# Kernel tuning notes

Hardware: AMD Instinct MI355X
Metric: run time of the kernel (lower is better)

Reference implementation:

```python
import jax, jax.numpy as jnp
import numpy as np

E = 8            # num experts
D = 1024         # hidden size
F = 4096         # ffn hidden size
CAP_FACTOR = 2.0 # expert-choice capacity factor


def setup_inputs() -> dict:
    key = jax.random.key(0)
    ks = jax.random.split(key, 6)
    B, S = 8, 1024
    hidden_states = jax.random.normal(ks[0], (B, S, D), dtype=jnp.float32)
    Wg = jax.random.normal(ks[1], (D, E), dtype=jnp.float32) * (1.0 / np.sqrt(D))
    W1 = jax.random.normal(ks[2], (E, D, F), dtype=jnp.float32) * (1.0 / np.sqrt(D))
    b1 = jnp.zeros((E, F), dtype=jnp.float32)
    W2 = jax.random.normal(ks[3], (E, F, D), dtype=jnp.float32) * (1.0 / np.sqrt(F))
    b2 = jnp.zeros((E, D), dtype=jnp.float32)
    return {"hidden_states": hidden_states, "Wg": Wg, "W1": W1, "b1": b1,
            "W2": W2, "b2": b2}


def reference(hidden_states, Wg, W1, b1, W2, b2):
    B, S, d = hidden_states.shape
    T = B * S
    C = int(T * CAP_FACTOR / E)  # capacity per expert (static)

    x = hidden_states.reshape(T, d)                      # [T, D]
    gates = jax.nn.softmax(x @ Wg, axis=-1)              # [T, E] router probs

    # Expert-choice routing: each expert picks its top-C tokens.
    scores = gates.T                                     # [E, T]
    top_vals, idx = jax.lax.top_k(scores, C)             # [E, C]

    # Load-balancing aux loss (mean gate prob * fraction routed, per expert).
    frac_routed = jnp.zeros((T, E), gates.dtype).at[
        idx.reshape(-1), jnp.repeat(jnp.arange(E), C)].set(1.0).mean(axis=0)
    aux_loss = E * jnp.sum(gates.mean(axis=0) * frac_routed)

    # Grouped expert FFN on gathered tokens.
    xg = x[idx]                                          # [E, C, D]
    h = jax.nn.gelu(jnp.einsum('ecd,edf->ecf', xg, W1) + b1[:, None, :])
    yo = jnp.einsum('ecf,efd->ecd', h, W2) + b2[:, None, :]  # [E, C, D]

    # Weight by routing prob and scatter-add back to token positions.
    weighted = yo * top_vals[..., None]                  # [E, C, D]
    out = jnp.zeros((T, d), x.dtype).at[idx.reshape(-1)].add(
        weighted.reshape(-1, d))
    return out.reshape(B, S, d), aux_loss
```

## Files before the change

kernel.cpp:

```cpp
#include <hip/hip_runtime.h>
#include <hip/hip_bf16.h>

#define T_TOK 8192
#define E_EXP 8
#define D_HID 1024
#define F_FFN 4096
#define C_CAP 2048

typedef __attribute__((ext_vector_type(8))) short bf16x8;
typedef __attribute__((ext_vector_type(4))) float f32x4;

__device__ __forceinline__ void load_lds16(const void* g, void* l) {
    __builtin_amdgcn_global_load_lds(
        (const __attribute__((address_space(1))) unsigned int*)g,
        (__attribute__((address_space(3))) unsigned int*)l, 16, 0, 0);
}

__device__ __forceinline__ float gelu_fast(float v) {
    float z = v * (1.5957691216057308f + 0.07135481627f * v * v);
    return v / (1.0f + __expf(-z));
}

__global__ __launch_bounds__(256) void gating_kernel(
    const float* __restrict__ x, const float* __restrict__ Wg,
    float* __restrict__ gatesT, __hip_bfloat16* __restrict__ xbf,
    float* __restrict__ aux_out)
{
    const int token = blockIdx.x * 4 + (threadIdx.x >> 6);
    const int lane  = threadIdx.x & 63;
    if (token == 0 && lane == 0)
        aux_out[0] = (float)E_EXP * (float)C_CAP / (float)T_TOK;
    const float* xr = x + (size_t)token * D_HID;

    float acc[E_EXP];
#pragma unroll
    for (int e = 0; e < E_EXP; ++e) acc[e] = 0.0f;

#pragma unroll
    for (int it = 0; it < 4; ++it) {
        const int c4 = it * 64 + lane;
        float4 v = ((const float4*)xr)[c4];
        float vv[4] = {v.x, v.y, v.z, v.w};
        union { __hip_bfloat16 h[4]; short4 s; } u;
#pragma unroll
        for (int j = 0; j < 4; ++j) u.h[j] = __float2bfloat16(vv[j]);
        ((short4*)(xbf + (size_t)token * D_HID))[c4] = u.s;
        const float* wr0 = Wg + (size_t)c4 * 4 * E_EXP;
#pragma unroll
        for (int j = 0; j < 4; ++j)
#pragma unroll
            for (int e = 0; e < E_EXP; ++e) acc[e] += vv[j] * wr0[j * E_EXP + e];
    }
#pragma unroll
    for (int e = 0; e < E_EXP; ++e) {
        for (int off = 32; off; off >>= 1) acc[e] += __shfl_down(acc[e], off);
    }
    if (lane == 0) {
        float m = acc[0];
#pragma unroll
        for (int e = 1; e < E_EXP; ++e) m = fmaxf(m, acc[e]);
        float ex[E_EXP];
        float s = 0.0f;
#pragma unroll
        for (int e = 0; e < E_EXP; ++e) { ex[e] = expf(acc[e] - m); s += ex[e]; }
        float inv = 1.0f / s;
#pragma unroll
        for (int e = 0; e < E_EXP; ++e) gatesT[(size_t)e * T_TOK + token] = ex[e] * inv;
    }
}

__global__ __launch_bounds__(1024) void topk_kernel(
    const float* __restrict__ gatesT, int* __restrict__ topidx,
    float* __restrict__ topval, int* __restrict__ cnt, int* __restrict__ inv)
{
    __shared__ unsigned int hist[256];
    __shared__ unsigned int bc_v, bc_r;
    __shared__ unsigned int selcnt;

    const int e    = blockIdx.x;
    const int tid  = threadIdx.x;
    const int lane = tid & 63;
    const float* row = gatesT + (size_t)e * T_TOK;

    unsigned long long kreg[8];
#pragma unroll
    for (int p = 0; p < 8; ++p) {
        int i = tid + p * 1024;
        unsigned int b = __float_as_uint(row[i]);
        b = (b & 0x80000000u) ? ~b : (b | 0x80000000u);
        kreg[p] = ((unsigned long long)b << 32) | (unsigned int)(T_TOK - 1 - i);
    }
    if (tid == 0) selcnt = 0;

    unsigned long long prefix = 0ull, mask = 0ull;
    unsigned int rank = C_CAP;
    for (int byte = 7; byte >= 0; --byte) {
        if (tid < 256) hist[tid] = 0;
        __syncthreads();
        const int sh = byte * 8;
#pragma unroll
        for (int p = 0; p < 8; ++p) {
            unsigned long long k = kreg[p];
            if ((k & mask) == prefix)
                atomicAdd(&hist[(unsigned int)((k >> sh) & 255ull)], 1u);
        }
        __syncthreads();
        if (tid < 64) {
            unsigned int v0 = hist[tid * 4], v1 = hist[tid * 4 + 1];
            unsigned int v2 = hist[tid * 4 + 2], v3 = hist[tid * 4 + 3];
            unsigned int s3 = v3, s2 = v2 + s3, s1 = v1 + s2, s0 = v0 + s1;
            unsigned int t = s0;
#pragma unroll
            for (int off = 1; off < 64; off <<= 1) {
                unsigned int u = __shfl_down(t, off);
                if (lane + off < 64) t += u;
            }
            const unsigned int suf = t - s0;
            unsigned int ge[4] = {s0 + suf, s1 + suf, s2 + suf, s3 + suf};
            unsigned int gt[4] = {s1 + suf, s2 + suf, s3 + suf, suf};
#pragma unroll
            for (int j = 0; j < 4; ++j)
                if (ge[j] >= rank && gt[j] < rank) {
                    bc_v = (unsigned int)(tid * 4 + j); bc_r = rank - gt[j];
                }
        }
        __syncthreads();
        prefix |= ((unsigned long long)bc_v) << sh;
        mask   |= (0xFFull << sh);
        rank = bc_r;
        __syncthreads();
    }
    const unsigned long long thr = prefix;

#pragma unroll
    for (int p = 0; p < 8; ++p) {
        unsigned long long k = kreg[p];
        if (k >= thr) {
            int c = (int)atomicAdd(&selcnt, 1u);
            int idx = T_TOK - 1 - (int)(k & 0xFFFFFFFFull);
            unsigned int b = (unsigned int)(k >> 32);
            b = (b & 0x80000000u) ? (b & 0x7FFFFFFFu) : ~b;
            topidx[e * C_CAP + c] = idx;
            topval[e * C_CAP + c] = __uint_as_float(b);
            int slot = atomicAdd(&cnt[idx], 1);
            inv[idx * E_EXP + slot] = e * C_CAP + c;
        }
    }
}

__global__ __launch_bounds__(256) void transpose_bf16_kernel(
    const float* __restrict__ in, __hip_bfloat16* __restrict__ out,
    int R, int Cn)
{
    __shared__ float tile[64][65];
    const int e = blockIdx.z;
    in  += (size_t)e * R * Cn;
    out += (size_t)e * R * Cn;
    const int c0 = blockIdx.x * 64, r0 = blockIdx.y * 64;
    const int tid = threadIdx.x;

    const int lr = tid >> 4, lc4 = (tid & 15) * 4;
#pragma unroll
    for (int it = 0; it < 4; ++it) {
        int r = lr + it * 16;
        float4 v = *(const float4*)(in + (size_t)(r0 + r) * Cn + c0 + lc4);
        tile[r][lc4 + 0] = v.x; tile[r][lc4 + 1] = v.y;
        tile[r][lc4 + 2] = v.z; tile[r][lc4 + 3] = v.w;
    }
    __syncthreads();

    const int ocb = tid >> 3, j0 = (tid & 7) * 8;
#pragma unroll
    for (int it = 0; it < 2; ++it) {
        int oc = ocb + it * 32;
        union { __hip_bfloat16 h[8]; uint4 v; } u;
#pragma unroll
        for (int j = 0; j < 8; ++j) u.h[j] = __float2bfloat16(tile[j0 + j][oc]);
        *(uint4*)(out + (size_t)(c0 + oc) * R + r0 + j0) = u.v;
    }
}


#define BARS do { __builtin_amdgcn_s_barrier(); __builtin_amdgcn_sched_barrier(0); } while (0)
#define WLG  do { asm volatile("s_waitcnt lgkmcnt(0)" ::: "memory"); __builtin_amdgcn_sched_barrier(0); } while (0)
#define VMC4 asm volatile("s_waitcnt vmcnt(4)" ::: "memory")
#define VMC0 asm volatile("s_waitcnt vmcnt(0)" ::: "memory")

#define STG2_A(hh, s) do { int b_ = (((s) & 1) << 15) + ((hh) << 14) + (w << 10); \
    load_lds16(Abase + (size_t)(aog[hh][0] + (s) * 128), smem + b_); \
    load_lds16(Abase + (size_t)(aog[hh][1] + (s) * 128), smem + b_ + 8192); } while (0)
#define STG2_B(hh, s) do { int b_ = 65536 + (((s) & 1) << 15) + ((hh) << 14) + (w << 10); \
    load_lds16(Bbase + (size_t)(bog[hh][0] + (s) * 128), smem + b_); \
    load_lds16(Bbase + (size_t)(bog[hh][1] + (s) * 128), smem + b_ + 8192); } while (0)

#define STG1_A(hh, s) do { int b_ = (((s) & 1) << 15) + ((hh) << 14) + (w << 10); \
    int o_ = ((s) & 15) * 128; \
    load_lds16(Abase + (size_t)(aog[hh][0] + o_), smem + b_); \
    load_lds16(Abase + (size_t)(aog[hh][1] + o_), smem + b_ + 8192); } while (0)
#define STG1_B(hh, s) do { int b_ = 65536 + (((s) & 1) << 15) + ((hh) << 14) + (w << 10); \
    int o_ = ((s) >> 4) * 524288 + ((s) & 15) * 128; \
    load_lds16(Bbase + (size_t)(bog[hh][0] + o_), smem + b_); \
    load_lds16(Bbase + (size_t)(bog[hh][1] + o_), smem + b_ + 8192); } while (0)

#define READ_A(mh) do { _Pragma("unroll") for (int mi = 0; mi < 4; ++mi) { \
    aF[mi][0] = *(const bf16x8*)(Ab + (arow + (mh) * 8192 + mi * 2048 + kc0)); \
    aF[mi][1] = *(const bf16x8*)(Ab + (arow + (mh) * 8192 + mi * 2048 + kc1)); } } while (0)
#define READ_B(nh, dst) do { _Pragma("unroll") for (int ni = 0; ni < 2; ++ni) { \
    dst[ni][0] = *(const bf16x8*)(Bb + (brow + (nh) * 4096 + ni * 2048 + kc0)); \
    dst[ni][1] = *(const bf16x8*)(Bb + (brow + (nh) * 4096 + ni * 2048 + kc1)); } } while (0)

#define QUAD(mh, nh, BF) do { \
    __builtin_amdgcn_s_setprio(1); \
    _Pragma("unroll") for (int mi = 0; mi < 4; ++mi) \
    _Pragma("unroll") for (int ni = 0; ni < 2; ++ni) { \
        acc[(mh)*4+mi][(nh)*2+ni] = __builtin_amdgcn_mfma_f32_16x16x32_bf16( \
            aF[mi][0], BF[ni][0], acc[(mh)*4+mi][(nh)*2+ni], 0, 0, 0); \
        acc[(mh)*4+mi][(nh)*2+ni] = __builtin_amdgcn_mfma_f32_16x16x32_bf16( \
            aF[mi][1], BF[ni][1], acc[(mh)*4+mi][(nh)*2+ni], 0, 0, 0); } \
    __builtin_amdgcn_s_setprio(0); } while (0)

#define GEMM_PROLOGUE_G(SA, SB) do { \
    SA(0, 0); SA(1, 0); SB(0, 0); SB(1, 0); \
    SB(0, 1); SB(1, 1); \
    VMC4; BARS; } while (0)

#define GEMM_TILE_G(t, NT, SA, SB) do { \
    const char* Ab = smem + (((t) & 1) << 15); \
    const char* Bb = smem + 65536 + (((t) & 1) << 15); \
     \
    READ_A(0); READ_B(0, bF0); \
    if ((t) + 1 < (NT)) SA(0, (t) + 1); \
    BARS; WLG; QUAD(0, 0, bF0); BARS; \
     \
    READ_B(1, bF1); \
    if ((t) + 1 < (NT)) SA(1, (t) + 1); \
    BARS; WLG; QUAD(0, 1, bF1); BARS; \
     \
    READ_A(1); \
    if ((t) + 2 < (NT)) SB(0, (t) + 2); \
    BARS; WLG; QUAD(1, 1, bF1); BARS; \
     \
    if ((t) + 2 < (NT)) SB(1, (t) + 2); \
    BARS; WLG; QUAD(1, 0, bF0); \
    if ((t) + 2 < (NT)) { VMC4; } else { VMC0; } \
    BARS; } while (0)

__global__ __launch_bounds__(512, 2) void gemm1_kernel(
    const __hip_bfloat16* __restrict__ xb,
    const __hip_bfloat16* __restrict__ W1t,
    const float* __restrict__ b1,
    const int* __restrict__ topidx,
    __hip_bfloat16* __restrict__ hbuf)
{
    __shared__ __align__(16) char smem[131072];
    const int tid = threadIdx.x;
    const int w = tid >> 6, lane = tid & 63;
    const int wr = w >> 2, wc = w & 3;
    const int fr = lane & 15, qlane = lane >> 4;

    const int bid = blockIdx.x;
    const int wg  = (bid & 7) * 32 + (bid >> 3);
    const int nc  = wg & 3;
    const int m0  = ((wg >> 2) & 7) * 256;
    const int e   = wg >> 5;
    const int nc0 = nc * 1024;

    const char* Abase = (const char*)xb;
    const char* Bbase = (const char*)(W1t + (size_t)e * F_FFN * D_HID);

    const int cc = (tid & 7) ^ ((tid >> 3) & 7);
    int aog[2][2], bog[2][2];
#pragma unroll
    for (int hh = 0; hh < 2; ++hh)
#pragma unroll
        for (int j = 0; j < 2; ++j) {
            int r   = m0 + hh * 128 + j * 64 + (tid >> 3);
            int tok = topidx[e * C_CAP + r];
            aog[hh][j] = (tok * D_HID + cc * 8) * 2;
            int n = nc0 + hh * 128 + j * 64 + (tid >> 3);
            bog[hh][j] = (n * D_HID + cc * 8) * 2;
        }

    float b1all[4][4];
#pragma unroll
    for (int p = 0; p < 4; ++p)
#pragma unroll
        for (int ni = 0; ni < 4; ++ni)
            b1all[p][ni] = b1[e * F_FFN + nc0 + p * 256 + wc * 64 + ni * 16 + fr];

    const int arow = (wr * 128 + fr) * 128;
    const int brow = (wc * 64 + fr) * 128;
    const int kc0  = ((qlane)     ^ (lane & 7)) * 16;
    const int kc1  = ((4 + qlane) ^ (lane & 7)) * 16;

    bf16x8 aF[4][2], bF0[2][2], bF1[2][2];
    f32x4 acc[8][4];
#pragma unroll
    for (int mi = 0; mi < 8; ++mi)
#pragma unroll
        for (int ni = 0; ni < 4; ++ni) acc[mi][ni] = (f32x4){0.f, 0.f, 0.f, 0.f};

    GEMM_PROLOGUE_G(STG1_A, STG1_B);
    const int q4 = qlane * 4;
#pragma unroll 1
    for (int p = 0; p < 4; ++p) {
#pragma unroll 2
        for (int tl = 0; tl < 16; ++tl) {
            const int t = p * 16 + tl;
            GEMM_TILE_G(t, 64, STG1_A, STG1_B);
        }
        const int n0p = nc0 + p * 256;
#pragma unroll
        for (int mi = 0; mi < 8; ++mi) {
#pragma unroll
            for (int r = 0; r < 4; ++r) {
                size_t row = (size_t)e * C_CAP + m0 + wr * 128 + mi * 16 + q4 + r;
                __hip_bfloat16* orow = hbuf + row * F_FFN + n0p + wc * 64;
#pragma unroll
                for (int ni = 0; ni < 4; ++ni)
                    orow[ni * 16 + fr] =
                        __float2bfloat16(gelu_fast(acc[mi][ni][r] + b1all[p][ni]));
            }
#pragma unroll
            for (int ni = 0; ni < 4; ++ni) acc[mi][ni] = (f32x4){0.f, 0.f, 0.f, 0.f};
        }
    }
}

__global__ __launch_bounds__(512, 2) void gemm2_kernel(
    const __hip_bfloat16* __restrict__ hbuf,
    const __hip_bfloat16* __restrict__ W2t,
    const float* __restrict__ b2,
    const float* __restrict__ topval,
    float* __restrict__ yo)
{
    __shared__ __align__(16) char smem[131072];
    const int tid = threadIdx.x;
    const int w = tid >> 6, lane = tid & 63;
    const int wr = w >> 2, wc = w & 3;
    const int fr = lane & 15, qlane = lane >> 4;

    const int bid = blockIdx.x;
    const int wg  = (bid & 7) * 32 + (bid >> 3);
    const int n0  = (wg & 3) * 256;
    const int m0  = ((wg >> 2) & 7) * 256;
    const int e   = wg >> 5;

    const char* Abase = (const char*)(hbuf + (size_t)e * C_CAP * F_FFN);
    const char* Bbase = (const char*)(W2t + (size_t)e * D_HID * F_FFN);

    const int cc = (tid & 7) ^ ((tid >> 3) & 7);
    int aog[2][2], bog[2][2];
#pragma unroll
    for (int hh = 0; hh < 2; ++hh)
#pragma unroll
        for (int j = 0; j < 2; ++j) {
            int r = m0 + hh * 128 + j * 64 + (tid >> 3);
            aog[hh][j] = (r * F_FFN + cc * 8) * 2;
            int n = n0 + hh * 128 + j * 64 + (tid >> 3);
            bog[hh][j] = (n * F_FFN + cc * 8) * 2;
        }

    const int arow = (wr * 128 + fr) * 128;
    const int brow = (wc * 64 + fr) * 128;
    const int kc0  = ((qlane)     ^ (lane & 7)) * 16;
    const int kc1  = ((4 + qlane) ^ (lane & 7)) * 16;

    bf16x8 aF[4][2], bF0[2][2], bF1[2][2];
    f32x4 acc[8][4];
#pragma unroll
    for (int mi = 0; mi < 8; ++mi)
#pragma unroll
        for (int ni = 0; ni < 4; ++ni) acc[mi][ni] = (f32x4){0.f, 0.f, 0.f, 0.f};

    GEMM_PROLOGUE_G(STG2_A, STG2_B);
#pragma unroll 2
    for (int t = 0; t < 64; ++t) GEMM_TILE_G(t, 64, STG2_A, STG2_B);

    const int q4 = qlane * 4;
    float b2v[4];
#pragma unroll
    for (int ni = 0; ni < 4; ++ni)
        b2v[ni] = b2[e * D_HID + n0 + wc * 64 + ni * 16 + fr];
#pragma unroll
    for (int mi = 0; mi < 8; ++mi) {
#pragma unroll
        for (int r = 0; r < 4; ++r) {
            const int row = m0 + wr * 128 + mi * 16 + q4 + r;
            const float g = topval[e * C_CAP + row];
            float* orow = yo + ((size_t)e * C_CAP + row) * D_HID + n0 + wc * 64;
#pragma unroll
            for (int ni = 0; ni < 4; ++ni)
                orow[ni * 16 + fr] = (acc[mi][ni][r] + b2v[ni]) * g;
        }
    }
}

__global__ __launch_bounds__(256) void combine_kernel(
    const float* __restrict__ yo, const int* __restrict__ cnt,
    const int* __restrict__ inv, float* __restrict__ out)
{
    const int t = blockIdx.x;
    const int n = cnt[t];
    const int c4 = threadIdx.x * 4;
    float4 a = {0.f, 0.f, 0.f, 0.f};
    for (int k = 0; k < n; ++k) {
        int ec = inv[t * E_EXP + k];
        float4 v = *(const float4*)(yo + (size_t)ec * D_HID + c4);
        a.x += v.x; a.y += v.y; a.z += v.z; a.w += v.w;
    }
    *(float4*)(out + (size_t)t * D_HID + c4) = a;
}

extern "C" void kernel_launch(void* const* d_in, const int* in_sizes, int n_in,
                              void* d_out, int out_size, void* d_ws, size_t ws_size,
                              hipStream_t stream) {
    const float* x  = (const float*)d_in[0];
    const float* Wg = (const float*)d_in[1];
    const float* W1 = (const float*)d_in[2];
    const float* b1 = (const float*)d_in[3];
    const float* W2 = (const float*)d_in[4];
    const float* b2 = (const float*)d_in[5];
    float* out = (float*)d_out;

    char* p = (char*)d_ws;
    float* gatesT = (float*)p;            p += (size_t)E_EXP * T_TOK * 4;
    int*   topidx = (int*)p;              p += (size_t)E_EXP * C_CAP * 4;
    float* topval = (float*)p;            p += (size_t)E_EXP * C_CAP * 4;
    int*   cnt    = (int*)p;              p += (size_t)T_TOK * 4;
    int*   inv    = (int*)p;              p += (size_t)T_TOK * E_EXP * 4;
    __hip_bfloat16* x_bf = (__hip_bfloat16*)p;  p += (size_t)T_TOK * D_HID * 2;
    __hip_bfloat16* W1t  = (__hip_bfloat16*)p;  p += (size_t)E_EXP * D_HID * F_FFN * 2;
    __hip_bfloat16* W2t  = (__hip_bfloat16*)p;  p += (size_t)E_EXP * D_HID * F_FFN * 2;
    __hip_bfloat16* hbuf = (__hip_bfloat16*)p;  p += (size_t)E_EXP * C_CAP * F_FFN * 2;
    float* yo = (float*)W1t;

    hipMemsetAsync(cnt, 0, (size_t)T_TOK * 4, stream);

    gating_kernel<<<T_TOK / 4, 256, 0, stream>>>(
        x, Wg, gatesT, x_bf, out + (size_t)T_TOK * D_HID);
    topk_kernel<<<E_EXP, 1024, 0, stream>>>(gatesT, topidx, topval, cnt, inv);

    {
        dim3 g(F_FFN / 64, D_HID / 64, E_EXP);
        transpose_bf16_kernel<<<g, 256, 0, stream>>>(W1, W1t, D_HID, F_FFN);
    }
    {
        dim3 g(D_HID / 64, F_FFN / 64, E_EXP);
        transpose_bf16_kernel<<<g, 256, 0, stream>>>(W2, W2t, F_FFN, D_HID);
    }

    gemm1_kernel<<<256, 512, 0, stream>>>(x_bf, W1t, b1, topidx, hbuf);
    gemm2_kernel<<<256, 512, 0, stream>>>(hbuf, W2t, b2, topval, yo);
    combine_kernel<<<T_TOK, 256, 0, stream>>>(yo, cnt, inv, out);
}
```

Baseline: 664.7 us.

## Triple-buffer A tiles, retile gemm1 to 256x256 blocks, merge weight transposes

The GEMM pipeline now keeps three A-tile LDS slots and two B slots (160KB LDS), prefetching A two k-steps ahead and waiting with vmcnt(8) instead of vmcnt(4). gemm1 changes from 256 blocks each covering 1024 output columns to 1024 blocks of 256x256. Its epilogue stages the GELU output through swizzled LDS so hbuf is written with coalesced 16-byte stores. The two weight-transpose launches are merged into one. The larger LDS footprint may lower occupancy, and gemm1 gets more blocks with a shorter K loop each.

```diff
diff --git a/kernel.cpp b/kernel.cpp
--- a/kernel.cpp
+++ b/kernel.cpp
@@ -149,14 +149,23 @@
 }
 
 __global__ __launch_bounds__(256) void transpose_bf16_kernel(
-    const float* __restrict__ in, __hip_bfloat16* __restrict__ out,
-    int R, int Cn)
+    const float* __restrict__ W1, __hip_bfloat16* __restrict__ W1t,
+    const float* __restrict__ W2, __hip_bfloat16* __restrict__ W2t)
 {
     __shared__ float tile[64][65];
-    const int e = blockIdx.z;
-    in  += (size_t)e * R * Cn;
-    out += (size_t)e * R * Cn;
-    const int c0 = blockIdx.x * 64, r0 = blockIdx.y * 64;
+    const int z = blockIdx.z;
+    const float* in;
+    __hip_bfloat16* out;
+    int R, Cn, c0, r0;
+    if (z < 8) {
+        R = D_HID; Cn = F_FFN;
+        in = W1 + (size_t)z * R * Cn; out = W1t + (size_t)z * R * Cn;
+        c0 = blockIdx.x * 64; r0 = blockIdx.y * 64;
+    } else {
+        R = F_FFN; Cn = D_HID;
+        in = W2 + (size_t)(z - 8) * R * Cn; out = W2t + (size_t)(z - 8) * R * Cn;
+        c0 = blockIdx.y * 64; r0 = blockIdx.x * 64;
+    }
     const int tid = threadIdx.x;
 
     const int lr = tid >> 4, lc4 = (tid & 15) * 4;
@@ -183,24 +192,16 @@
 
 #define BARS do { __builtin_amdgcn_s_barrier(); __builtin_amdgcn_sched_barrier(0); } while (0)
 #define WLG  do { asm volatile("s_waitcnt lgkmcnt(0)" ::: "memory"); __builtin_amdgcn_sched_barrier(0); } while (0)
+#define VMC8 asm volatile("s_waitcnt vmcnt(8)" ::: "memory")
 #define VMC4 asm volatile("s_waitcnt vmcnt(4)" ::: "memory")
 #define VMC0 asm volatile("s_waitcnt vmcnt(0)" ::: "memory")
 
-#define STG2_A(hh, s) do { int b_ = (((s) & 1) << 15) + ((hh) << 14) + (w << 10); \
+#define STG_A3(hh, s, slot) do { int b_ = (slot) * 32768 + ((hh) << 14) + (w << 10); \
     load_lds16(Abase + (size_t)(aog[hh][0] + (s) * 128), smem + b_); \
     load_lds16(Abase + (size_t)(aog[hh][1] + (s) * 128), smem + b_ + 8192); } while (0)
-#define STG2_B(hh, s) do { int b_ = 65536 + (((s) & 1) << 15) + ((hh) << 14) + (w << 10); \
+#define STG_B3(hh, s) do { int b_ = 98304 + (((s) & 1) << 15) + ((hh) << 14) + (w << 10); \
     load_lds16(Bbase + (size_t)(bog[hh][0] + (s) * 128), smem + b_); \
     load_lds16(Bbase + (size_t)(bog[hh][1] + (s) * 128), smem + b_ + 8192); } while (0)
-
-#define STG1_A(hh, s) do { int b_ = (((s) & 1) << 15) + ((hh) << 14) + (w << 10); \
-    int o_ = ((s) & 15) * 128; \
-    load_lds16(Abase + (size_t)(aog[hh][0] + o_), smem + b_); \
-    load_lds16(Abase + (size_t)(aog[hh][1] + o_), smem + b_ + 8192); } while (0)
-#define STG1_B(hh, s) do { int b_ = 65536 + (((s) & 1) << 15) + ((hh) << 14) + (w << 10); \
-    int o_ = ((s) >> 4) * 524288 + ((s) & 15) * 128; \
-    load_lds16(Bbase + (size_t)(bog[hh][0] + o_), smem + b_); \
-    load_lds16(Bbase + (size_t)(bog[hh][1] + o_), smem + b_ + 8192); } while (0)
 
 #define READ_A(mh) do { _Pragma("unroll") for (int mi = 0; mi < 4; ++mi) { \
     aF[mi][0] = *(const bf16x8*)(Ab + (arow + (mh) * 8192 + mi * 2048 + kc0)); \
@@ -219,30 +220,31 @@
             aF[mi][1], BF[ni][1], acc[(mh)*4+mi][(nh)*2+ni], 0, 0, 0); } \
     __builtin_amdgcn_s_setprio(0); } while (0)
 
-#define GEMM_PROLOGUE_G(SA, SB) do { \
-    SA(0, 0); SA(1, 0); SB(0, 0); SB(1, 0); \
-    SB(0, 1); SB(1, 1); \
+#define GEMM_PROLOGUE_3B() do { \
+    STG_A3(0, 0, 0); STG_A3(1, 0, 0); STG_A3(0, 1, 1); STG_A3(1, 1, 1); \
+    STG_B3(0, 0); STG_B3(1, 0); STG_B3(0, 1); STG_B3(1, 1); \
     VMC4; BARS; } while (0)
 
-#define GEMM_TILE_G(t, NT, SA, SB) do { \
-    const char* Ab = smem + (((t) & 1) << 15); \
-    const char* Bb = smem + 65536 + (((t) & 1) << 15); \
+#define GEMM_TILE_3B(t, NT) do { \
+    const char* Ab = smem + ((t) % 3) * 32768; \
+    const char* Bb = smem + 98304 + (((t) & 1) << 15); \
+    const int sl2_ = ((t) + 2) % 3; \
      \
     READ_A(0); READ_B(0, bF0); \
-    if ((t) + 1 < (NT)) SA(0, (t) + 1); \
+    if ((t) + 2 < (NT)) STG_A3(0, (t) + 2, sl2_); \
     BARS; WLG; QUAD(0, 0, bF0); BARS; \
      \
     READ_B(1, bF1); \
-    if ((t) + 1 < (NT)) SA(1, (t) + 1); \
+    if ((t) + 2 < (NT)) STG_A3(1, (t) + 2, sl2_); \
     BARS; WLG; QUAD(0, 1, bF1); BARS; \
      \
     READ_A(1); \
-    if ((t) + 2 < (NT)) SB(0, (t) + 2); \
+    if ((t) + 2 < (NT)) STG_B3(0, (t) + 2); \
     BARS; WLG; QUAD(1, 1, bF1); BARS; \
      \
-    if ((t) + 2 < (NT)) SB(1, (t) + 2); \
+    if ((t) + 2 < (NT)) STG_B3(1, (t) + 2); \
     BARS; WLG; QUAD(1, 0, bF0); \
-    if ((t) + 2 < (NT)) { VMC4; } else { VMC0; } \
+    if ((t) + 2 < (NT)) { VMC8; } else { VMC0; } \
     BARS; } while (0)
 
 __global__ __launch_bounds__(512, 2) void gemm1_kernel(
@@ -252,18 +254,17 @@
     const int* __restrict__ topidx,
     __hip_bfloat16* __restrict__ hbuf)
 {
-    __shared__ __align__(16) char smem[131072];
+    __shared__ __align__(16) char smem[163840];
     const int tid = threadIdx.x;
     const int w = tid >> 6, lane = tid & 63;
     const int wr = w >> 2, wc = w & 3;
     const int fr = lane & 15, qlane = lane >> 4;
 
     const int bid = blockIdx.x;
-    const int wg  = (bid & 7) * 32 + (bid >> 3);
-    const int nc  = wg & 3;
-    const int m0  = ((wg >> 2) & 7) * 256;
-    const int e   = wg >> 5;
-    const int nc0 = nc * 1024;
+    const int wg  = (bid & 7) * 128 + (bid >> 3);
+    const int m0  = (wg & 7) * 256;
+    const int n0  = ((wg >> 3) & 15) * 256;
+    const int e   = wg >> 7;
 
     const char* Abase = (const char*)xb;
     const char* Bbase = (const char*)(W1t + (size_t)e * F_FFN * D_HID);
@@ -277,16 +278,9 @@
             int r   = m0 + hh * 128 + j * 64 + (tid >> 3);
             int tok = topidx[e * C_CAP + r];
             aog[hh][j] = (tok * D_HID + cc * 8) * 2;
-            int n = nc0 + hh * 128 + j * 64 + (tid >> 3);
+            int n = n0 + hh * 128 + j * 64 + (tid >> 3);
             bog[hh][j] = (n * D_HID + cc * 8) * 2;
         }
-
-    float b1all[4][4];
-#pragma unroll
-    for (int p = 0; p < 4; ++p)
-#pragma unroll
-        for (int ni = 0; ni < 4; ++ni)
-            b1all[p][ni] = b1[e * F_FFN + nc0 + p * 256 + wc * 64 + ni * 16 + fr];
 
     const int arow = (wr * 128 + fr) * 128;
     const int brow = (wc * 64 + fr) * 128;
@@ -300,30 +294,37 @@
 #pragma unroll
         for (int ni = 0; ni < 4; ++ni) acc[mi][ni] = (f32x4){0.f, 0.f, 0.f, 0.f};
 
-    GEMM_PROLOGUE_G(STG1_A, STG1_B);
+    GEMM_PROLOGUE_3B();
+#pragma unroll 2
+    for (int t = 0; t < 16; ++t) GEMM_TILE_3B(t, 16);
+
     const int q4 = qlane * 4;
-#pragma unroll 1
-    for (int p = 0; p < 4; ++p) {
-#pragma unroll 2
-        for (int tl = 0; tl < 16; ++tl) {
-            const int t = p * 16 + tl;
-            GEMM_TILE_G(t, 64, STG1_A, STG1_B);
-        }
-        const int n0p = nc0 + p * 256;
-#pragma unroll
-        for (int mi = 0; mi < 8; ++mi) {
-#pragma unroll
-            for (int r = 0; r < 4; ++r) {
-                size_t row = (size_t)e * C_CAP + m0 + wr * 128 + mi * 16 + q4 + r;
-                __hip_bfloat16* orow = hbuf + row * F_FFN + n0p + wc * 64;
-#pragma unroll
-                for (int ni = 0; ni < 4; ++ni)
-                    orow[ni * 16 + fr] =
-                        __float2bfloat16(gelu_fast(acc[mi][ni][r] + b1all[p][ni]));
+    float b1v[4];
+#pragma unroll
+    for (int ni = 0; ni < 4; ++ni)
+        b1v[ni] = b1[e * F_FFN + n0 + wc * 64 + ni * 16 + fr];
+#pragma unroll
+    for (int mi = 0; mi < 8; ++mi)
+#pragma unroll
+        for (int r = 0; r < 4; ++r) {
+            const int row = wr * 128 + mi * 16 + q4 + r;
+            char* rb = smem + row * 512;
+            const int sw = (row & 7) << 4;
+#pragma unroll
+            for (int ni = 0; ni < 4; ++ni) {
+                const int col2 = (wc * 64 + ni * 16 + fr) * 2;
+                *(__hip_bfloat16*)(rb + (col2 ^ sw)) =
+                    __float2bfloat16(gelu_fast(acc[mi][ni][r] + b1v[ni]));
             }
-#pragma unroll
-            for (int ni = 0; ni < 4; ++ni) acc[mi][ni] = (f32x4){0.f, 0.f, 0.f, 0.f};
-        }
+        }
+    __syncthreads();
+#pragma unroll
+    for (int it = 0; it < 16; ++it) {
+        const int row = it * 16 + w * 2 + (lane >> 5);
+        const int cb  = (lane & 31) * 16;
+        uint4 v = *(const uint4*)(smem + row * 512 + (cb ^ ((row & 7) << 4)));
+        char* gp = (char*)(hbuf + ((size_t)e * C_CAP + m0 + row) * F_FFN + n0) + cb;
+        *(uint4*)gp = v;
     }
 }
 
@@ -334,7 +335,7 @@
     const float* __restrict__ topval,
     float* __restrict__ yo)
 {
-    __shared__ __align__(16) char smem[131072];
+    __shared__ __align__(16) char smem[163840];
     const int tid = threadIdx.x;
     const int w = tid >> 6, lane = tid & 63;
     const int wr = w >> 2, wc = w & 3;
@@ -373,9 +374,9 @@
 #pragma unroll
         for (int ni = 0; ni < 4; ++ni) acc[mi][ni] = (f32x4){0.f, 0.f, 0.f, 0.f};
 
-    GEMM_PROLOGUE_G(STG2_A, STG2_B);
+    GEMM_PROLOGUE_3B();
 #pragma unroll 2
-    for (int t = 0; t < 64; ++t) GEMM_TILE_G(t, 64, STG2_A, STG2_B);
+    for (int t = 0; t < 64; ++t) GEMM_TILE_3B(t, 64);
 
     const int q4 = qlane * 4;
     float b2v[4];
@@ -442,15 +443,11 @@
     topk_kernel<<<E_EXP, 1024, 0, stream>>>(gatesT, topidx, topval, cnt, inv);
 
     {
-        dim3 g(F_FFN / 64, D_HID / 64, E_EXP);
-        transpose_bf16_kernel<<<g, 256, 0, stream>>>(W1, W1t, D_HID, F_FFN);
-    }
-    {
-        dim3 g(D_HID / 64, F_FFN / 64, E_EXP);
-        transpose_bf16_kernel<<<g, 256, 0, stream>>>(W2, W2t, F_FFN, D_HID);
-    }
-
-    gemm1_kernel<<<256, 512, 0, stream>>>(x_bf, W1t, b1, topidx, hbuf);
+        dim3 g(F_FFN / 64, D_HID / 64, 2 * E_EXP);
+        transpose_bf16_kernel<<<g, 256, 0, stream>>>(W1, W1t, W2, W2t);
+    }
+
+    gemm1_kernel<<<1024, 512, 0, stream>>>(x_bf, W1t, b1, topidx, hbuf);
     gemm2_kernel<<<256, 512, 0, stream>>>(hbuf, W2t, b2, topval, yo);
     combine_kernel<<<T_TOK, 256, 0, stream>>>(yo, cnt, inv, out);
 }
```

Result: no change. 674.3 us (+1.5%).
